# Kernel optimization log

Hardware: AMD Instinct MI355X
Metric: run time of the kernel (lower is better)

The kernel has to match this reference:

```python
import jax, jax.numpy as jnp
import numpy as np

B, K, D, E = 8192, 5, 128, 128
QD = D + 1              # query_dim = embedding_dimension + time_encoding_dim(=1)
KD = K * (D + E + 1)    # flattened neighborhood feature width = key_dim*5


def setup_inputs() -> dict:
    key = jax.random.key(0)
    ks = jax.random.split(key, 20)
    n = jax.random.normal
    u = jax.random.uniform
    return {
        # hop-2 neighborhood (neighbors-of-neighbors of B roots)
        "emb0": n(ks[0], (B * K, K, D), jnp.float32),
        "ef0": n(ks[1], (B * K, K, E), jnp.float32),
        "td0": u(ks[2], (B * K, K, 1), jnp.float32),
        # hop-1 neighborhood
        "emb1": n(ks[3], (B, K, D), jnp.float32),
        "ef1": n(ks[4], (B, K, E), jnp.float32),
        "td1": u(ks[5], (B, K, 1), jnp.float32),
        # root embeddings
        "emb2": n(ks[6], (B, D), jnp.float32),
        # single-head MultiheadAttention params (q/k/v in-proj + out-proj)
        "Wq": n(ks[7], (QD, QD), jnp.float32) * 0.05,
        "bq": jnp.zeros((QD,), jnp.float32),
        "Wk": n(ks[8], (QD, KD), jnp.float32) * 0.02,
        "bk": jnp.zeros((QD,), jnp.float32),
        "Wv": n(ks[9], (QD, KD), jnp.float32) * 0.02,
        "bv": jnp.zeros((QD,), jnp.float32),
        "Wo": n(ks[10], (QD, QD), jnp.float32) * 0.05,
        "bo": jnp.zeros((QD,), jnp.float32),
        # fc1: (query_dim + D) -> D, fc2: D -> D
        "W1": n(ks[11], (D, QD + D), jnp.float32) * 0.05,
        "b1": jnp.zeros((D,), jnp.float32),
        "W2": n(ks[12], (D, D), jnp.float32) * 0.05,
        "b2": jnp.zeros((D,), jnp.float32),
    }


def reference(emb0, ef0, td0, emb1, ef1, td1, emb2,
              Wq, bq, Wk, bk, Wv, bv, Wo, bo, W1, b1, W2, b2):
    def attn(q, kv):
        # single-head MHA, batch_first; PyTorch scales q by head_dim**-0.5
        qp = (q @ Wq.T + bq) * (1.0 / jnp.sqrt(jnp.asarray(QD, q.dtype)))
        kp = kv @ Wk.T + bk
        vp = kv @ Wv.T + bv
        w = jax.nn.softmax(jnp.einsum("bqd,bkd->bqk", qp, kp), axis=-1)
        o = jnp.einsum("bqk,bkd->bqd", w, vp)
        return o @ Wo.T + bo

    def mlp(x):
        return jax.nn.relu(x @ W1.T + b1) @ W2.T + b2

    # i = 0: hop-2 neighborhoods attend into hop-1 nodes
    nf0 = jnp.concatenate([emb0, ef0, td0], axis=-1).reshape(B, K, KD)  # [B,K,KD]
    q0 = jnp.concatenate([emb1, td1], axis=-1)                          # [B,K,QD]
    a0 = attn(q0, nf0)
    r0 = mlp(jnp.concatenate([a0, emb1], axis=-1))                      # [B,K,D]

    # i = 1 (last): hop-1 neighborhoods; 2-D root query is reshaped to [1,B,QD]
    # so attention runs across the whole batch, as in the original code.
    nf1 = jnp.concatenate([emb1, ef1, td1], axis=-1).reshape(1, B, KD)  # [1,B,KD]
    q1 = jnp.concatenate([emb2, jnp.zeros((B, 1), emb2.dtype)], axis=-1)[None]
    a1 = attn(q1, nf1)
    r1 = mlp(jnp.concatenate([a1, emb2[None]], axis=-1))[0]             # [B,D]

    return (r0, r1)
```

## Files before the change

kernel.cpp:

```cpp
#include <hip/hip_runtime.h>

#define B_   8192
#define K_   5
#define D_   128
#define QD_  129
#define KD_  1285
#define SQ_  132
#define BK_  40960
#define QPAD 160
#define VPAD 144
#define KDP  1312

typedef unsigned short u16;
typedef unsigned int   u32;
typedef __attribute__((ext_vector_type(8))) short bf8_t;
typedef __attribute__((ext_vector_type(4))) float f4_t;
typedef __attribute__((address_space(3))) u32 lds_u32;
typedef __attribute__((address_space(1))) const u32 glob_u32;

#define MFMA16(a, b, c) __builtin_amdgcn_mfma_f32_16x16x32_bf16(a, b, c, 0, 0, 0)

__device__ __forceinline__ u16 f2bf(float x) {
  u32 u = __float_as_uint(x);
  u = (u + 0x7fffu + ((u >> 16) & 1u)) >> 16;
  return (u16)u;
}
__device__ __forceinline__ float bf2f(u16 v) {
  return __uint_as_float((u32)v << 16);
}
__device__ __forceinline__ u32 pack2(float a, float b) {
  return (u32)f2bf(a) | ((u32)f2bf(b) << 16);
}
__device__ __forceinline__ float exp2_fast(float x) {
#if __has_builtin(__builtin_amdgcn_exp2f)
  return __builtin_amdgcn_exp2f(x);
#else
  float r; asm("v_exp_f32 %0, %1" : "=v"(r) : "v"(x)); return r;
#endif
}
__device__ __forceinline__ u32 cvtpk(float a, float b) {
  u32 r;
  asm("v_cvt_pk_bf16_f32 %0, %1, %2" : "=v"(r) : "v"(a), "v"(b));
  return r;
}
__device__ __forceinline__ int swz8(int row, int seg) {
  return (row << 5) + (((seg ^ (row >> 1)) & 3) << 3);
}
__device__ __forceinline__ void gload16(const u16* src, u16* ldsdst) {
  __builtin_amdgcn_global_load_lds((glob_u32*)src, (lds_u32*)ldsdst, 16, 0, 0);
}
#define WAIT_VM0() asm volatile("s_waitcnt vmcnt(0)" ::: "memory")
#define WAIT_VM3() asm volatile("s_waitcnt vmcnt(3)" ::: "memory")
#define WAIT_VM4() asm volatile("s_waitcnt vmcnt(4)" ::: "memory")
#define WAIT_VM6() asm volatile("s_waitcnt vmcnt(6)" ::: "memory")
#define WAIT_LGKM0() asm volatile("s_waitcnt lgkmcnt(0)" ::: "memory")

__global__ __launch_bounds__(256) void convw_k(
    const float* __restrict__ Wq, const float* __restrict__ Wk,
    const float* __restrict__ Wv, const float* __restrict__ Wo,
    const float* __restrict__ W1, const float* __restrict__ W2,
    u16* __restrict__ wb)
{
  int idx = blockIdx.x * 256 + threadIdx.x;
  if (idx < 377856) {
    int r = idx / KDP, c = idx - r * KDP;
    float v = 0.f;
    if (c < KD_) {
      if (r < 129) v = Wk[r * KD_ + c];
      else if (r < 258) v = Wv[(r - 129) * KD_ + c];
    }
    wb[idx] = f2bf(v);
    return;
  }
  int i2 = idx - 377856;
  if (i2 < 23040) {
    int r = i2 / 160, c = i2 - r * 160;
    wb[idx] = f2bf((r < 129 && c < 129) ? Wq[r * 129 + c] : 0.f);
    return;
  }
  i2 -= 23040;
  if (i2 < 23040) {
    int r = i2 / 160, c = i2 - r * 160;
    wb[idx] = f2bf((r < 129 && c < 129) ? Wo[r * 129 + c] : 0.f);
    return;
  }
  i2 -= 23040;
  if (i2 < 41472) {
    int r = i2 / 288, c = i2 - r * 288;
    wb[idx] = f2bf((r < 128 && c < 257) ? W1[r * 257 + c] : 0.f);
    return;
  }
  i2 -= 41472;
  if (i2 < 18432) {
    int r = i2 / 128, c = i2 - r * 128;
    wb[idx] = f2bf(r < 128 ? W2[r * 128 + c] : 0.f);
  }
}

__global__ __launch_bounds__(256) void packnf_k(
    const float* __restrict__ emb, const float* __restrict__ ef,
    const float* __restrict__ td, u16* __restrict__ dst, int nofs, int rows)
{
  int idx = blockIdx.x * 256 + threadIdx.x;
  if (idx >= rows * 328) return;
  int nr = idx / 328, q = idx - nr * 328;
  const int n = nofs + nr;
  const int c0 = q * 4;
  u16 o[4];
#pragma unroll
  for (int i = 0; i < 4; ++i) {
    int c = c0 + i;
    float v = 0.f;
    if (c < KD_) {
      int j = c / 257, r = c - j * 257;
      int base = (n * 5 + j) << 7;
      v = (r < 128) ? emb[base + r] : (r < 256) ? ef[base + r - 128] : td[n * 5 + j];
    }
    o[i] = f2bf(v);
  }
  *(uint2*)&dst[(size_t)nr * KDP + c0] = *(const uint2*)o;
}

template<int GA, bool RELU, int OM0, int OM1, bool DUAL>
__global__ __launch_bounds__(256) void gmm_k(
    int nK, int Kw, int nch,
    const void* __restrict__ A, int ast,
    const float* __restrict__ g1, const float* __restrict__ g2,
    const u16* __restrict__ Wb,
    const float* __restrict__ b0, void* __restrict__ out0, int ost0, int N0,
    const float* __restrict__ b1, void* __restrict__ out1, int ost1,
    float scale)
{
  __shared__ u16 Ws_[3][9 * 512];
  const int t = threadIdx.x, lane = t & 63, w = t >> 6;
  const int lrow = lane & 15, lk = lane >> 4;
  const int bid = blockIdx.x;
  const int x = bid / nch, colh = bid - x * nch;
  const int n0 = x * 64;
  const int colofs = colh * 144;
  const int drow = lane >> 2, dseg = lane & 3;
  const int arow = n0 + w * 16 + lrow;

  f4_t acc[9];
#pragma unroll
  for (int ct = 0; ct < 9; ++ct) acc[ct] = (f4_t){0.f, 0.f, 0.f, 0.f};

  bf8_t afE, afO;
  float rE[8], rO[8];

  auto issueR = [&](int kst, float (&r)[8]) {
    const int cb = kst * 32 + lk * 8;
#pragma unroll
    for (int i = 0; i < 8; ++i) {
      int c = cb + i;
      uintptr_t pa = (uintptr_t)((const float*)A + (arow << 7) + c);
      uintptr_t pt = (uintptr_t)(g2 ? (g2 + arow) : (const float*)A);
      uintptr_t sel = (c < 128) ? pa : pt;
      float v = *(const float*)sel;
      r[i] = (c < 128) ? v : ((c == 128 && g2) ? v : 0.f);
    }
  };
  auto cvt8 = [&](const float (&r)[8]) -> bf8_t {
    union { bf8_t v; u32 u[4]; } xx;
#pragma unroll
    for (int i = 0; i < 4; ++i) xx.u[i] = pack2(r[2 * i], r[2 * i + 1]);
    return xx.v;
  };
  auto loadAf = [&](int kst) -> bf8_t {
    return *(const bf8_t*)((const u16*)A + (size_t)arow * ast + kst * 32 + lk * 8);
  };
  auto dmaW = [&](int kst, u16* wbuf) {
    const int c0 = kst * 32;
#pragma unroll
    for (int si = 0; si < 3; ++si) {
      int s = w + si * 4;
      if (s < 9) {
        int rr = colofs + s * 16 + drow;
        int sseg = (dseg ^ (rr >> 1)) & 3;
        gload16(&Wb[(size_t)rr * Kw + c0 + sseg * 8], wbuf + s * 512);
      }
    }
  };
  auto compute = [&](bf8_t af, const u16* wsb) {
#pragma unroll
    for (int ct = 0; ct < 9; ++ct) {
      bf8_t bf = *(const bf8_t*)&wsb[swz8(ct * 16 + lrow, lk)];
      acc[ct] = MFMA16(af, bf, acc[ct]);
    }
  };

  if constexpr (GA == 0) {
    u16 *wa = Ws_[0], *wbuf = Ws_[1], *wc = Ws_[2];
    afE = loadAf(0);
    dmaW(0, wa);
    if (nK > 1) { afO = loadAf(1); dmaW(1, wbuf); }
    if (nK > 1) { WAIT_VM4(); } else { WAIT_VM0(); }
    __builtin_amdgcn_s_barrier();
    int k = 0;
    while (true) {
      if (k + 2 < nK) dmaW(k + 2, wc);
      compute(afE, wa);
      if (k + 2 < nK) afE = loadAf(k + 2);
      if (k + 1 >= nK) break;
      if (k + 2 < nK) { WAIT_VM4(); } else { WAIT_VM0(); }
      __builtin_amdgcn_s_barrier();
      { u16* tp = wa; wa = wbuf; wbuf = wc; wc = tp; }
      ++k;
      if (k + 2 < nK) dmaW(k + 2, wc);
      compute(afO, wa);
      if (k + 2 < nK) afO = loadAf(k + 2);
      if (k + 1 >= nK) break;
      if (k + 2 < nK) { WAIT_VM4(); } else { WAIT_VM0(); }
      __builtin_amdgcn_s_barrier();
      { u16* tp = wa; wa = wbuf; wbuf = wc; wc = tp; }
      ++k;
    }
  } else {
    issueR(0, rE);
    dmaW(0, Ws_[0]);
    WAIT_VM0();
    afE = cvt8(rE);
    __builtin_amdgcn_s_barrier();
    int cur = 0, k = 0;
    while (true) {
      if (k + 1 < nK) { issueR(k + 1, rO); dmaW(k + 1, Ws_[cur ^ 1]); }
      compute(afE, Ws_[cur]);
      if (k + 1 >= nK) break;
      WAIT_VM0();
      afO = cvt8(rO);
      __builtin_amdgcn_s_barrier();
      cur ^= 1; ++k;
      if (k + 1 < nK) { issueR(k + 1, rE); dmaW(k + 1, Ws_[cur ^ 1]); }
      compute(afO, Ws_[cur]);
      if (k + 1 >= nK) break;
      WAIT_VM0();
      afE = cvt8(rE);
      __builtin_amdgcn_s_barrier();
      cur ^= 1; ++k;
    }
  }

#pragma unroll
  for (int ct = 0; ct < 9; ++ct) {
    const int col = colofs + ct * 16 + lrow;
#pragma unroll
    for (int r = 0; r < 4; ++r) {
      const int n = n0 + w * 16 + lk * 4 + r;
      float v = acc[ct][r];
      if (col < N0) {
        v = (v + b0[col]) * scale;
        if (RELU) v = fmaxf(v, 0.f);
        if (OM0 == 0)      ((float*)out0)[(size_t)n * ost0 + col] = v;
        else if (OM0 == 1) ((u16*)out0)[(size_t)n * ost0 + col] = f2bf(v);
        else               ((u16*)out0)[(size_t)col * ost0 + n] = f2bf(v);
      } else if (DUAL) {
        int o = col - N0;
        if (o < 129) {
          v = (v + b1[o]) * scale;
          if (RELU) v = fmaxf(v, 0.f);
          if (OM1 == 0)      ((float*)out1)[(size_t)n * ost1 + o] = v;
          else if (OM1 == 1) ((u16*)out1)[(size_t)n * ost1 + o] = f2bf(v);
          else               ((u16*)out1)[(size_t)o * ost1 + n] = f2bf(v);
        }
      }
    }
  }
}

__global__ __launch_bounds__(256) void embpack_k(
    const float* __restrict__ src, u16* __restrict__ dst, int rows)
{
  int idx = blockIdx.x * 256 + threadIdx.x;
  if (idx >= rows * 128) return;
  int n = idx >> 7, c = idx & 127;
  dst[(size_t)n * 288 + 129 + c] = f2bf(src[idx]);
}

__global__ __launch_bounds__(256) void attn0_k(
    const u16* __restrict__ qp, const u16* __restrict__ kp,
    const u16* __restrict__ vp, u16* __restrict__ o0b)
{
  __shared__ float qs[4][5][SQ_], ks[4][5][SQ_], vs[4][5][SQ_];
  __shared__ float ps[4][5][8];
  const int t = threadIdx.x;
  const int bbase = blockIdx.x * 4;
  for (int idx = t; idx < 4 * 5 * 33; idx += 256) {
    int bl = idx / 165;
    int rem = idx - bl * 165;
    int row = rem / 33;
    int g = rem - row * 33;
    int n = (bbase + bl) * 5 + row;
    int d0 = g * 4;
    uint2 uq = *(const uint2*)&qp[(size_t)n * 160 + d0];
    uint2 uk = *(const uint2*)&kp[(size_t)n * 160 + d0];
    uint2 uv = *(const uint2*)&vp[(size_t)n * 160 + d0];
    u16 eq[4] = {(u16)uq.x, (u16)(uq.x >> 16), (u16)uq.y, (u16)(uq.y >> 16)};
    u16 ek[4] = {(u16)uk.x, (u16)(uk.x >> 16), (u16)uk.y, (u16)(uk.y >> 16)};
    u16 ev[4] = {(u16)uv.x, (u16)(uv.x >> 16), (u16)uv.y, (u16)(uv.y >> 16)};
#pragma unroll
    for (int i = 0; i < 4; ++i) {
      int d = d0 + i;
      bool ok = d < QD_;
      qs[bl][row][d] = ok ? bf2f(eq[i]) : 0.f;
      ks[bl][row][d] = ok ? bf2f(ek[i]) : 0.f;
      vs[bl][row][d] = ok ? bf2f(ev[i]) : 0.f;
    }
  }
  __syncthreads();
  const int w = t >> 6, lane = t & 63;
  if (lane < 25) {
    int qq = lane / 5, kk = lane - (lane / 5) * 5;
    float s = 0.f;
    for (int c = 0; c < SQ_; c += 4) {
      float4 qv = *(const float4*)&qs[w][qq][c];
      float4 kv = *(const float4*)&ks[w][kk][c];
      s += qv.x * kv.x + qv.y * kv.y + qv.z * kv.z + qv.w * kv.w;
    }
    ps[w][qq][kk] = s;
  }
  __syncthreads();
  if (lane < 5) {
    float m = -1e30f;
#pragma unroll
    for (int k = 0; k < 5; ++k) m = fmaxf(m, ps[w][lane][k]);
    float l = 0.f; float e[5];
#pragma unroll
    for (int k = 0; k < 5; ++k) { e[k] = __expf(ps[w][lane][k] - m); l += e[k]; }
    float inv = 1.f / l;
#pragma unroll
    for (int k = 0; k < 5; ++k) ps[w][lane][k] = e[k] * inv;
  }
  __syncthreads();
  for (int d = lane; d < 160; d += 64) {
#pragma unroll
    for (int qq = 0; qq < 5; ++qq) {
      float o = 0.f;
      if (d < QD_) {
#pragma unroll
        for (int k = 0; k < 5; ++k) o += ps[w][qq][k] * vs[w][k][d];
      }
      o0b[(size_t)((bbase + w) * 5 + qq) * 160 + d] = f2bf(o);
    }
  }
}

#define QB   128
#define KVB  64
#define NSPLIT 8
#define NT   ((B_ / NSPLIT) / KVB)
__global__ __launch_bounds__(512, 4) void flashm_k(
    const u16* __restrict__ qp, const u16* __restrict__ kp,
    const u16* __restrict__ vpT, float* __restrict__ oacc,
    float* __restrict__ marr, float* __restrict__ larr)
{
  __shared__ u16 Ks[2][5 * 2048];
  __shared__ u16 Vs[2 * 4608];
  __shared__ u16 Ps[2 * 4096];
  const int t = threadIdx.x, lane = t & 63, w = t >> 6;
  const int lrow = lane & 15, lk = lane >> 4;
  const int split = blockIdx.x & (NSPLIT - 1);
  const int q0 = (blockIdx.x >> 3) * QB;
  const int drow = lane >> 2, dseg = lane & 3;
  const int kbase = split * (B_ / NSPLIT);

  auto dmaK = [&](int k0, u16* kb) {
#pragma unroll
    for (int si = 0; si < 3; ++si) {
      int s = w + si * 8;
      if (s >= 20) s -= 20;
      int kst = s >> 2, rg = s & 3;
      int r = rg * 16 + drow;
      int sseg = (dseg ^ (r >> 1)) & 3;
      gload16(&kp[(size_t)(k0 + r) * QPAD + kst * 32 + sseg * 8],
              kb + kst * 2048 + rg * 512);
    }
  };
  auto dmaV = [&](int k0) {
#pragma unroll
    for (int si = 0; si < 3; ++si) {
      int s = w + si * 8;
      if (s >= 18) s -= 18;
      int kst = (s >= 9) ? 1 : 0;
      int rg = s - kst * 9;
      int r = rg * 16 + drow;
      int sseg = (dseg ^ (r >> 1)) & 3;
      gload16(&vpT[(size_t)r * B_ + k0 + kst * 32 + sseg * 8],
              Vs + kst * 4608 + rg * 512);
    }
  };

  bf8_t qf[5];
  {
    const u16* qrow = qp + (size_t)(q0 + w * 16 + lrow) * QPAD;
#pragma unroll
    for (int kst = 0; kst < 5; ++kst)
      qf[kst] = *(const bf8_t*)(qrow + kst * 32 + lk * 8);
  }

  f4_t acc[9];
#pragma unroll
  for (int ct = 0; ct < 9; ++ct) acc[ct] = (f4_t){0.f, 0.f, 0.f, 0.f};
  float m_[4] = {-1e30f, -1e30f, -1e30f, -1e30f};
  float l_[4] = {0.f, 0.f, 0.f, 0.f};

  dmaK(kbase, Ks[0]);
  for (int tl = 0; tl < NT; ++tl) {
    const int k0 = kbase + tl * KVB;
    const int cur = tl & 1;
    dmaV(k0);
    const bool more = (tl + 1 < NT);
    if (more) dmaK(k0 + KVB, Ks[cur ^ 1]);
    if (more) { WAIT_VM6(); } else { WAIT_VM3(); }
    __builtin_amdgcn_s_barrier();

    f4_t s4[4];
#pragma unroll
    for (int ct = 0; ct < 4; ++ct) s4[ct] = (f4_t){0.f, 0.f, 0.f, 0.f};
#pragma unroll
    for (int kst = 0; kst < 5; ++kst) {
#pragma unroll
      for (int ct = 0; ct < 4; ++ct) {
        bf8_t b = *(const bf8_t*)&Ks[cur][kst * 2048 + swz8(ct * 16 + lrow, lk)];
        s4[ct] = MFMA16(qf[kst], b, s4[ct]);
      }
    }

    float lmax[4];
#pragma unroll
    for (int r = 0; r < 4; ++r)
      lmax[r] = fmaxf(fmaxf(s4[0][r], s4[1][r]), fmaxf(s4[2][r], s4[3][r]));
    bool need = (lmax[0] > m_[0] + 8.f) || (lmax[1] > m_[1] + 8.f) ||
                (lmax[2] > m_[2] + 8.f) || (lmax[3] > m_[3] + 8.f);
    if (__any(need)) {
      float cf[4];
#pragma unroll
      for (int r = 0; r < 4; ++r) {
        float pm = lmax[r];
#pragma unroll
        for (int mk = 1; mk <= 8; mk <<= 1) pm = fmaxf(pm, __shfl_xor(pm, mk));
        float mn = fmaxf(m_[r], pm);
        cf[r] = exp2_fast(m_[r] - mn);
        m_[r] = mn;
        l_[r] *= cf[r];
      }
#pragma unroll
      for (int ct = 0; ct < 9; ++ct) {
#pragma unroll
        for (int r = 0; r < 4; ++r) acc[ct][r] *= cf[r];
      }
    }
    float pv[4][4];
#pragma unroll
    for (int ct = 0; ct < 4; ++ct) {
#pragma unroll
      for (int r = 0; r < 4; ++r) {
        pv[ct][r] = exp2_fast(s4[ct][r] - m_[r]);
        l_[r] += pv[ct][r];
      }
    }
#pragma unroll
    for (int half = 0; half < 2; ++half) {
#pragma unroll
      for (int r = 0; r < 4; ++r) {
        u32 pk = cvtpk(pv[half * 2][r], pv[half * 2 + 1][r]);
        const int q = w * 16 + lk * 4 + r;
        const int c0 = lrow, c1 = 16 + lrow;
        const int base = half * 4096 + (q << 5);
        Ps[base + ((((c0 >> 3) ^ (q >> 1)) & 3) << 3) + (c0 & 7)] = (u16)pk;
        Ps[base + ((((c1 >> 3) ^ (q >> 1)) & 3) << 3) + (c1 & 7)] = (u16)(pk >> 16);
      }
    }
    WAIT_LGKM0();
    __builtin_amdgcn_sched_barrier(0);

    if (more) { WAIT_VM3(); } else { WAIT_VM0(); }
    __builtin_amdgcn_s_barrier();

#pragma unroll
    for (int kst = 0; kst < 2; ++kst) {
      bf8_t a = *(const bf8_t*)&Ps[kst * 4096 + swz8(w * 16 + lrow, lk)];
#pragma unroll
      for (int ct = 0; ct < 9; ++ct) {
        bf8_t b = *(const bf8_t*)&Vs[kst * 4608 + swz8(ct * 16 + lrow, lk)];
        acc[ct] = MFMA16(a, b, acc[ct]);
      }
    }
    __builtin_amdgcn_s_barrier();
  }

#pragma unroll
  for (int r = 0; r < 4; ++r) {
#pragma unroll
    for (int mk = 1; mk <= 8; mk <<= 1) l_[r] += __shfl_xor(l_[r], mk);
  }

#pragma unroll
  for (int ct = 0; ct < 9; ++ct) {
    const int col = ct * 16 + lrow;
    if (col < SQ_) {
#pragma unroll
      for (int r = 0; r < 4; ++r)
        oacc[((size_t)split * B_ + q0 + w * 16 + lk * 4 + r) * SQ_ + col] = acc[ct][r];
    }
  }
  if (lrow == 0) {
#pragma unroll
    for (int r = 0; r < 4; ++r) {
      size_t i = (size_t)split * B_ + q0 + w * 16 + lk * 4 + r;
      marr[i] = m_[r];
      larr[i] = l_[r];
    }
  }
}

__global__ __launch_bounds__(256) void combine_k(
    const float* __restrict__ oacc, const float* __restrict__ marr,
    const float* __restrict__ larr, u16* __restrict__ o1b)
{
  int idx = blockIdx.x * 256 + threadIdx.x;
  if (idx >= B_ * 160) return;
  int n = idx / 160, d = idx - n * 160;
  float v = 0.f;
  if (d < QD_) {
    float m = -1e30f;
#pragma unroll
    for (int s = 0; s < NSPLIT; ++s) m = fmaxf(m, marr[s * B_ + n]);
    float l = 0.f, o = 0.f;
#pragma unroll
    for (int s = 0; s < NSPLIT; ++s) {
      float e = exp2_fast(marr[s * B_ + n] - m);
      l += larr[s * B_ + n] * e;
      o += oacc[((size_t)s * B_ + n) * SQ_ + d] * e;
    }
    v = o / l;
  }
  o1b[idx] = f2bf(v);
}

extern "C" void kernel_launch(void* const* d_in, const int* in_sizes, int n_in,
                              void* d_out, int out_size, void* d_ws, size_t ws_size,
                              hipStream_t stream)
{
  const float* emb0 = (const float*)d_in[0];
  const float* ef0  = (const float*)d_in[1];
  const float* td0  = (const float*)d_in[2];
  const float* emb1 = (const float*)d_in[3];
  const float* ef1  = (const float*)d_in[4];
  const float* td1  = (const float*)d_in[5];
  const float* emb2 = (const float*)d_in[6];
  const float* Wq = (const float*)d_in[7];  const float* bq = (const float*)d_in[8];
  const float* Wk = (const float*)d_in[9];  const float* bk = (const float*)d_in[10];
  const float* Wv = (const float*)d_in[11]; const float* bv = (const float*)d_in[12];
  const float* Wo = (const float*)d_in[13]; const float* bo = (const float*)d_in[14];
  const float* W1 = (const float*)d_in[15]; const float* b1 = (const float*)d_in[16];
  const float* W2 = (const float*)d_in[17]; const float* b2 = (const float*)d_in[18];
  float* out = (float*)d_out;

  char* ws = (char*)d_ws;
  u16* wb   = (u16*)ws;
  u16* wkv  = wb;
  u16* wq_b = wb + 377856;
  u16* wo_b = wb + 400896;
  u16* w1_b = wb + 423936;
  u16* w2_b = wb + 465408;
  u16*   kp0b = (u16*)(ws + 1048576);
  u16*   vp0b = (u16*)(ws + 14155776);
  u16*   qp0b = (u16*)(ws + 27262976);
  u16*   nfp  = (u16*)(ws + 44302336);
  u16*   o0b  = (u16*)(ws + 65929216);
  u16*   cat0 = (u16*)(ws + 1048576);
  u16*   h0   = (u16*)(ws + 24641536);
  u16*   nf1p = (u16*)(ws + 1048576);
  u16*   qp1b = (u16*)(ws + 22675456);
  u16*   kp1b = (u16*)(ws + 25296896);
  u16*   vp1T = (u16*)(ws + 27918336);
  u16*   o1b  = (u16*)(ws + 30277632);
  float* marr = (float*)(ws + 32899072);
  float* larr = (float*)(ws + 33161216);
  u16*   cat1 = (u16*)(ws + 33423360);
  u16*   h1   = (u16*)(ws + 38141952);
  float* oacc = (float*)(ws + 40239104);

  const float scale = 0.08804509063256238f;
  const float scale2 = scale * 1.4426950408889634f;
  const int HROWS = 20480;

  convw_k<<<1890, 256, 0, stream>>>(Wq, Wk, Wv, Wo, W1, W2, wb);

  for (int h = 0; h < 2; ++h) {
    packnf_k<<<(HROWS * 328 + 255) / 256, 256, 0, stream>>>(
        emb0, ef0, td0, nfp, h * HROWS, HROWS);
    gmm_k<0, false, 1, 1, true><<<(HROWS / 64) * 2, 256, 0, stream>>>(
        41, KDP, 2, nfp, KDP, nullptr, nullptr, wkv,
        bk, kp0b + (size_t)h * HROWS * 160, 160, QD_,
        bv, vp0b + (size_t)h * HROWS * 160, 160, 1.f);
  }
  gmm_k<1, false, 1, 0, false><<<640, 256, 0, stream>>>(
      5, 160, 1, emb1, 0, nullptr, td1, wq_b,
      bq, qp0b, 160, QD_, nullptr, nullptr, 0, scale);
  attn0_k<<<B_ / 4, 256, 0, stream>>>(qp0b, kp0b, vp0b, o0b);
  hipMemsetAsync(cat0, 0, 23592960, stream);
  embpack_k<<<(BK_ * 128 + 255) / 256, 256, 0, stream>>>(emb1, cat0, BK_);
  gmm_k<0, false, 1, 0, false><<<640, 256, 0, stream>>>(
      5, 160, 1, o0b, 160, nullptr, nullptr, wo_b,
      bo, cat0, 288, QD_, nullptr, nullptr, 0, 1.f);
  gmm_k<0, true, 1, 0, false><<<640, 256, 0, stream>>>(
      9, 288, 1, cat0, 288, nullptr, nullptr, w1_b,
      b1, h0, 128, 128, nullptr, nullptr, 0, 1.f);
  gmm_k<0, false, 0, 0, false><<<640, 256, 0, stream>>>(
      4, 128, 1, h0, 128, nullptr, nullptr, w2_b,
      b2, out, 128, 128, nullptr, nullptr, 0, 1.f);

  packnf_k<<<(B_ * 328 + 255) / 256, 256, 0, stream>>>(
      emb1, ef1, td1, nf1p, 0, B_);
  hipMemsetAsync(qp1b, 0, 2621440, stream);
  hipMemsetAsync(kp1b, 0, 2621440, stream);
  hipMemsetAsync(vp1T, 0, 2359296, stream);
  gmm_k<0, false, 1, 2, true><<<(B_ / 64) * 2, 256, 0, stream>>>(
      41, KDP, 2, nf1p, KDP, nullptr, nullptr, wkv,
      bk, kp1b, QPAD, QD_, bv, vp1T, B_, 1.f);
  gmm_k<1, false, 1, 0, false><<<128, 256, 0, stream>>>(
      5, 160, 1, emb2, 0, nullptr, nullptr, wq_b,
      bq, qp1b, QPAD, QD_, nullptr, nullptr, 0, scale2);
  flashm_k<<<(B_ / QB) * NSPLIT, 512, 0, stream>>>(qp1b, kp1b, vp1T, oacc, marr, larr);
  combine_k<<<(B_ * 160 + 255) / 256, 256, 0, stream>>>(oacc, marr, larr, o1b);
  hipMemsetAsync(cat1, 0, 4718592, stream);
  embpack_k<<<(B_ * 128 + 255) / 256, 256, 0, stream>>>(emb2, cat1, B_);
  gmm_k<0, false, 1, 0, false><<<128, 256, 0, stream>>>(
      5, 160, 1, o1b, 160, nullptr, nullptr, wo_b,
      bo, cat1, 288, QD_, nullptr, nullptr, 0, 1.f);
  gmm_k<0, true, 1, 0, false><<<128, 256, 0, stream>>>(
      9, 288, 1, cat1, 288, nullptr, nullptr, w1_b,
      b1, h1, 128, 128, nullptr, nullptr, 0, 1.f);
  gmm_k<0, false, 0, 0, false><<<128, 256, 0, stream>>>(
      4, 128, 1, h1, 128, nullptr, nullptr, w2_b,
      b2, out + (size_t)BK_ * D_, 128, 128, nullptr, nullptr, 0, 1.f);
}
```

Baseline: 416.2 us.

## Fuse concat into fc1 GEMM and rewrite flash attention with 32x32 MFMA

The fc1 GEMM now reads its A operand from two sources: the bf16 attention output (padded to 160) and the fp32 embeddings, converting the latter on the fly. This removes the memset and embpack kernels that used to build the concatenated buffer, and the W1 layout is repacked to 320 columns to match. Separately, the cross-batch flash attention kernel moves from 16x16x32 MFMA with 512-thread blocks to 32x32x16 MFMA with 256-thread blocks and 32 query rows per wave, giving more reuse per instruction. The cost is higher register pressure (16 row stats per lane) and a wider K step in fc1.

```diff
diff --git a/kernel.cpp b/kernel.cpp
--- a/kernel.cpp
+++ b/kernel.cpp
@@ -8,17 +8,18 @@
 #define SQ_  132
 #define BK_  40960
 #define QPAD 160
-#define VPAD 144
 #define KDP  1312
 
 typedef unsigned short u16;
 typedef unsigned int   u32;
 typedef __attribute__((ext_vector_type(8))) short bf8_t;
 typedef __attribute__((ext_vector_type(4))) float f4_t;
+typedef __attribute__((ext_vector_type(16))) float f16f;
 typedef __attribute__((address_space(3))) u32 lds_u32;
 typedef __attribute__((address_space(1))) const u32 glob_u32;
 
 #define MFMA16(a, b, c) __builtin_amdgcn_mfma_f32_16x16x32_bf16(a, b, c, 0, 0, 0)
+#define MFMA32(a, b, c) __builtin_amdgcn_mfma_f32_32x32x16_bf16(a, b, c, 0, 0, 0)
 
 __device__ __forceinline__ u16 f2bf(float x) {
   u32 u = __float_as_uint(x);
@@ -32,11 +33,7 @@
   return (u32)f2bf(a) | ((u32)f2bf(b) << 16);
 }
 __device__ __forceinline__ float exp2_fast(float x) {
-#if __has_builtin(__builtin_amdgcn_exp2f)
-  return __builtin_amdgcn_exp2f(x);
-#else
   float r; asm("v_exp_f32 %0, %1" : "=v"(r) : "v"(x)); return r;
-#endif
 }
 __device__ __forceinline__ u32 cvtpk(float a, float b) {
   u32 r;
@@ -50,9 +47,9 @@
   __builtin_amdgcn_global_load_lds((glob_u32*)src, (lds_u32*)ldsdst, 16, 0, 0);
 }
 #define WAIT_VM0() asm volatile("s_waitcnt vmcnt(0)" ::: "memory")
-#define WAIT_VM3() asm volatile("s_waitcnt vmcnt(3)" ::: "memory")
 #define WAIT_VM4() asm volatile("s_waitcnt vmcnt(4)" ::: "memory")
-#define WAIT_VM6() asm volatile("s_waitcnt vmcnt(6)" ::: "memory")
+#define WAIT_VM5() asm volatile("s_waitcnt vmcnt(5)" ::: "memory")
+#define WAIT_VM10() asm volatile("s_waitcnt vmcnt(10)" ::: "memory")
 #define WAIT_LGKM0() asm volatile("s_waitcnt lgkmcnt(0)" ::: "memory")
 
 __global__ __launch_bounds__(256) void convw_k(
@@ -85,12 +82,17 @@
     return;
   }
   i2 -= 23040;
-  if (i2 < 41472) {
-    int r = i2 / 288, c = i2 - r * 288;
-    wb[idx] = f2bf((r < 128 && c < 257) ? W1[r * 257 + c] : 0.f);
+  if (i2 < 46080) {
+    int r = i2 / 320, c = i2 - r * 320;
+    float v = 0.f;
+    if (r < 128) {
+      if (c < 129) v = W1[r * 257 + c];
+      else if (c >= 160 && c < 288) v = W1[r * 257 + (c - 31)];
+    }
+    wb[idx] = f2bf(v);
     return;
   }
-  i2 -= 41472;
+  i2 -= 46080;
   if (i2 < 18432) {
     int r = i2 / 128, c = i2 - r * 128;
     wb[idx] = f2bf(r < 128 ? W2[r * 128 + c] : 0.f);
@@ -121,7 +123,7 @@
   *(uint2*)&dst[(size_t)nr * KDP + c0] = *(const uint2*)o;
 }
 
-template<int GA, bool RELU, int OM0, int OM1, bool DUAL>
+template<int GA, bool RELU, int OM0, int OM1, bool DUAL, bool ZF = false>
 __global__ __launch_bounds__(256) void gmm_k(
     int nK, int Kw, int nch,
     const void* __restrict__ A, int ast,
@@ -145,7 +147,7 @@
 #pragma unroll
   for (int ct = 0; ct < 9; ++ct) acc[ct] = (f4_t){0.f, 0.f, 0.f, 0.f};
 
-  bf8_t afE, afO;
+  bf8_t afE, afO, dE, dO;
   float rE[8], rO[8];
 
   auto issueR = [&](int kst, float (&r)[8]) {
@@ -168,6 +170,22 @@
   };
   auto loadAf = [&](int kst) -> bf8_t {
     return *(const bf8_t*)((const u16*)A + (size_t)arow * ast + kst * 32 + lk * 8);
+  };
+  auto issue2 = [&](int kst, bf8_t& d, float (&r)[8]) {
+    if (GA == 1) { issueR(kst, r); return; }
+    if (kst < 5) { d = loadAf(kst); }
+    else if (kst < 9) {
+      const float* p = g1 + (size_t)arow * 128 + (kst - 5) * 32 + lk * 8;
+      *(float4*)&r[0] = *(const float4*)p;
+      *(float4*)&r[4] = *(const float4*)(p + 4);
+    }
+  };
+  auto finish2 = [&](int kst, bf8_t& d, float (&r)[8]) -> bf8_t {
+    if (GA == 1) return cvt8(r);
+    if (kst < 5) return d;
+    if (kst < 9) return cvt8(r);
+    bf8_t z = {0, 0, 0, 0, 0, 0, 0, 0};
+    return z;
   };
   auto dmaW = [&](int kst, u16* wbuf) {
     const int c0 = kst * 32;
@@ -216,25 +234,25 @@
       ++k;
     }
   } else {
-    issueR(0, rE);
+    issue2(0, dE, rE);
     dmaW(0, Ws_[0]);
     WAIT_VM0();
-    afE = cvt8(rE);
+    afE = finish2(0, dE, rE);
     __builtin_amdgcn_s_barrier();
     int cur = 0, k = 0;
     while (true) {
-      if (k + 1 < nK) { issueR(k + 1, rO); dmaW(k + 1, Ws_[cur ^ 1]); }
+      if (k + 1 < nK) { issue2(k + 1, dO, rO); dmaW(k + 1, Ws_[cur ^ 1]); }
       compute(afE, Ws_[cur]);
       if (k + 1 >= nK) break;
       WAIT_VM0();
-      afO = cvt8(rO);
+      afO = finish2(k + 1, dO, rO);
       __builtin_amdgcn_s_barrier();
       cur ^= 1; ++k;
-      if (k + 1 < nK) { issueR(k + 1, rE); dmaW(k + 1, Ws_[cur ^ 1]); }
+      if (k + 1 < nK) { issue2(k + 1, dE, rE); dmaW(k + 1, Ws_[cur ^ 1]); }
       compute(afO, Ws_[cur]);
       if (k + 1 >= nK) break;
       WAIT_VM0();
-      afE = cvt8(rE);
+      afE = finish2(k + 1, dE, rE);
       __builtin_amdgcn_s_barrier();
       cur ^= 1; ++k;
     }
@@ -262,18 +280,11 @@
           else if (OM1 == 1) ((u16*)out1)[(size_t)n * ost1 + o] = f2bf(v);
           else               ((u16*)out1)[(size_t)o * ost1 + n] = f2bf(v);
         }
+      } else if (ZF && col < 144) {
+        if (OM0 == 1) ((u16*)out0)[(size_t)n * ost0 + col] = 0;
       }
     }
   }
-}
-
-__global__ __launch_bounds__(256) void embpack_k(
-    const float* __restrict__ src, u16* __restrict__ dst, int rows)
-{
-  int idx = blockIdx.x * 256 + threadIdx.x;
-  if (idx >= rows * 128) return;
-  int n = idx >> 7, c = idx & 127;
-  dst[(size_t)n * 288 + 129 + c] = f2bf(src[idx]);
 }
 
 __global__ __launch_bounds__(256) void attn0_k(
@@ -348,16 +359,16 @@
 #define KVB  64
 #define NSPLIT 8
 #define NT   ((B_ / NSPLIT) / KVB)
-__global__ __launch_bounds__(512, 4) void flashm_k(
+__global__ __launch_bounds__(256, 2) void flashm_k(
     const u16* __restrict__ qp, const u16* __restrict__ kp,
     const u16* __restrict__ vpT, float* __restrict__ oacc,
     float* __restrict__ marr, float* __restrict__ larr)
 {
   __shared__ u16 Ks[2][5 * 2048];
-  __shared__ u16 Vs[2 * 4608];
-  __shared__ u16 Ps[2 * 4096];
+  __shared__ u16 Vs[2 * 5120];
+  __shared__ u16 Ps[4 * 2048];
   const int t = threadIdx.x, lane = t & 63, w = t >> 6;
-  const int lrow = lane & 15, lk = lane >> 4;
+  const int l31 = lane & 31, lh = lane >> 5;
   const int split = blockIdx.x & (NSPLIT - 1);
   const int q0 = (blockIdx.x >> 3) * QB;
   const int drow = lane >> 2, dseg = lane & 3;
@@ -365,9 +376,8 @@
 
   auto dmaK = [&](int k0, u16* kb) {
 #pragma unroll
-    for (int si = 0; si < 3; ++si) {
-      int s = w + si * 8;
-      if (s >= 20) s -= 20;
+    for (int si = 0; si < 5; ++si) {
+      int s = w + si * 4;
       int kst = s >> 2, rg = s & 3;
       int r = rg * 16 + drow;
       int sseg = (dseg ^ (r >> 1)) & 3;
@@ -377,31 +387,41 @@
   };
   auto dmaV = [&](int k0) {
 #pragma unroll
-    for (int si = 0; si < 3; ++si) {
-      int s = w + si * 8;
+    for (int si = 0; si < 5; ++si) {
+      int s = w + si * 4;
       if (s >= 18) s -= 18;
       int kst = (s >= 9) ? 1 : 0;
       int rg = s - kst * 9;
       int r = rg * 16 + drow;
       int sseg = (dseg ^ (r >> 1)) & 3;
       gload16(&vpT[(size_t)r * B_ + k0 + kst * 32 + sseg * 8],
-              Vs + kst * 4608 + rg * 512);
-    }
-  };
-
-  bf8_t qf[5];
+              Vs + kst * 5120 + rg * 512);
+    }
+  };
+
+  bf8_t qf[10];
   {
-    const u16* qrow = qp + (size_t)(q0 + w * 16 + lrow) * QPAD;
-#pragma unroll
-    for (int kst = 0; kst < 5; ++kst)
-      qf[kst] = *(const bf8_t*)(qrow + kst * 32 + lk * 8);
-  }
-
-  f4_t acc[9];
-#pragma unroll
-  for (int ct = 0; ct < 9; ++ct) acc[ct] = (f4_t){0.f, 0.f, 0.f, 0.f};
-  float m_[4] = {-1e30f, -1e30f, -1e30f, -1e30f};
-  float l_[4] = {0.f, 0.f, 0.f, 0.f};
+    const u16* qrow = qp + (size_t)(q0 + w * 32 + l31) * QPAD;
+#pragma unroll
+    for (int kst = 0; kst < 10; ++kst)
+      qf[kst] = *(const bf8_t*)(qrow + kst * 16 + lh * 8);
+  }
+
+  f16f acc[5];
+#pragma unroll
+  for (int ct = 0; ct < 5; ++ct)
+#pragma unroll
+    for (int j = 0; j < 16; ++j) acc[ct][j] = 0.f;
+  float m_[16], l_[16];
+#pragma unroll
+  for (int r = 0; r < 16; ++r) { m_[r] = -1e30f; l_[r] = 0.f; }
+
+  int paddr[16];
+#pragma unroll
+  for (int r = 0; r < 16; ++r) {
+    int q = (r & 3) + 8 * (r >> 2) + 4 * lh;
+    paddr[r] = w * 2048 + (q << 5) + ((((l31 >> 3) ^ (q >> 1)) & 3) << 3) + (l31 & 7);
+  }
 
   dmaK(kbase, Ks[0]);
   for (int tl = 0; tl < NT; ++tl) {
@@ -410,103 +430,92 @@
     dmaV(k0);
     const bool more = (tl + 1 < NT);
     if (more) dmaK(k0 + KVB, Ks[cur ^ 1]);
-    if (more) { WAIT_VM6(); } else { WAIT_VM3(); }
+    if (more) { WAIT_VM10(); } else { WAIT_VM5(); }
     __builtin_amdgcn_s_barrier();
 
-    f4_t s4[4];
-#pragma unroll
-    for (int ct = 0; ct < 4; ++ct) s4[ct] = (f4_t){0.f, 0.f, 0.f, 0.f};
-#pragma unroll
-    for (int kst = 0; kst < 5; ++kst) {
-#pragma unroll
-      for (int ct = 0; ct < 4; ++ct) {
-        bf8_t b = *(const bf8_t*)&Ks[cur][kst * 2048 + swz8(ct * 16 + lrow, lk)];
-        s4[ct] = MFMA16(qf[kst], b, s4[ct]);
+    f16f s0, s1;
+#pragma unroll
+    for (int j = 0; j < 16; ++j) { s0[j] = 0.f; s1[j] = 0.f; }
+#pragma unroll
+    for (int kst = 0; kst < 10; ++kst) {
+      const int seg = ((kst & 1) << 1) + lh;
+      bf8_t b0 = *(const bf8_t*)&Ks[cur][(kst >> 1) * 2048 + swz8(l31, seg)];
+      bf8_t b1 = *(const bf8_t*)&Ks[cur][(kst >> 1) * 2048 + swz8(32 + l31, seg)];
+      s0 = MFMA32(qf[kst], b0, s0);
+      s1 = MFMA32(qf[kst], b1, s1);
+    }
+
+    float lm[16];
+    bool need = false;
+#pragma unroll
+    for (int r = 0; r < 16; ++r) {
+      lm[r] = fmaxf(s0[r], s1[r]);
+      need = need || (lm[r] > m_[r] + 8.f);
+    }
+    if (__any(need)) {
+#pragma unroll
+      for (int r = 0; r < 16; ++r) {
+        float pm = lm[r];
+#pragma unroll
+        for (int mk = 1; mk <= 16; mk <<= 1) pm = fmaxf(pm, __shfl_xor(pm, mk));
+        float mn = fmaxf(m_[r], pm);
+        float cf = exp2_fast(m_[r] - mn);
+        m_[r] = mn;
+        l_[r] *= cf;
+#pragma unroll
+        for (int ct = 0; ct < 5; ++ct) acc[ct][r] *= cf;
       }
     }
-
-    float lmax[4];
-#pragma unroll
-    for (int r = 0; r < 4; ++r)
-      lmax[r] = fmaxf(fmaxf(s4[0][r], s4[1][r]), fmaxf(s4[2][r], s4[3][r]));
-    bool need = (lmax[0] > m_[0] + 8.f) || (lmax[1] > m_[1] + 8.f) ||
-                (lmax[2] > m_[2] + 8.f) || (lmax[3] > m_[3] + 8.f);
-    if (__any(need)) {
-      float cf[4];
-#pragma unroll
-      for (int r = 0; r < 4; ++r) {
-        float pm = lmax[r];
-#pragma unroll
-        for (int mk = 1; mk <= 8; mk <<= 1) pm = fmaxf(pm, __shfl_xor(pm, mk));
-        float mn = fmaxf(m_[r], pm);
-        cf[r] = exp2_fast(m_[r] - mn);
-        m_[r] = mn;
-        l_[r] *= cf[r];
-      }
-#pragma unroll
-      for (int ct = 0; ct < 9; ++ct) {
-#pragma unroll
-        for (int r = 0; r < 4; ++r) acc[ct][r] *= cf[r];
-      }
-    }
-    float pv[4][4];
-#pragma unroll
-    for (int ct = 0; ct < 4; ++ct) {
-#pragma unroll
-      for (int r = 0; r < 4; ++r) {
-        pv[ct][r] = exp2_fast(s4[ct][r] - m_[r]);
-        l_[r] += pv[ct][r];
-      }
-    }
-#pragma unroll
-    for (int half = 0; half < 2; ++half) {
-#pragma unroll
-      for (int r = 0; r < 4; ++r) {
-        u32 pk = cvtpk(pv[half * 2][r], pv[half * 2 + 1][r]);
-        const int q = w * 16 + lk * 4 + r;
-        const int c0 = lrow, c1 = 16 + lrow;
-        const int base = half * 4096 + (q << 5);
-        Ps[base + ((((c0 >> 3) ^ (q >> 1)) & 3) << 3) + (c0 & 7)] = (u16)pk;
-        Ps[base + ((((c1 >> 3) ^ (q >> 1)) & 3) << 3) + (c1 & 7)] = (u16)(pk >> 16);
-      }
+#pragma unroll
+    for (int r = 0; r < 16; ++r) {
+      float p0 = exp2_fast(s0[r] - m_[r]);
+      float p1 = exp2_fast(s1[r] - m_[r]);
+      l_[r] += p0 + p1;
+      u32 pk = cvtpk(p0, p1);
+      Ps[paddr[r]] = (u16)pk;
+      Ps[paddr[r] + 1024] = (u16)(pk >> 16);
     }
     WAIT_LGKM0();
     __builtin_amdgcn_sched_barrier(0);
 
-    if (more) { WAIT_VM3(); } else { WAIT_VM0(); }
+    if (more) { WAIT_VM5(); } else { WAIT_VM0(); }
     __builtin_amdgcn_s_barrier();
 
 #pragma unroll
-    for (int kst = 0; kst < 2; ++kst) {
-      bf8_t a = *(const bf8_t*)&Ps[kst * 4096 + swz8(w * 16 + lrow, lk)];
-#pragma unroll
-      for (int ct = 0; ct < 9; ++ct) {
-        bf8_t b = *(const bf8_t*)&Vs[kst * 4608 + swz8(ct * 16 + lrow, lk)];
-        acc[ct] = MFMA16(a, b, acc[ct]);
+    for (int kst = 0; kst < 4; ++kst) {
+      const int seg = ((kst & 1) << 1) + lh;
+      bf8_t a = *(const bf8_t*)&Ps[w * 2048 + (kst >> 1) * 1024 + swz8(l31, seg)];
+#pragma unroll
+      for (int ct = 0; ct < 5; ++ct) {
+        bf8_t b = *(const bf8_t*)&Vs[(kst >> 1) * 5120 + swz8(ct * 32 + l31, seg)];
+        acc[ct] = MFMA32(a, b, acc[ct]);
       }
     }
     __builtin_amdgcn_s_barrier();
   }
 
 #pragma unroll
-  for (int r = 0; r < 4; ++r) {
-#pragma unroll
-    for (int mk = 1; mk <= 8; mk <<= 1) l_[r] += __shfl_xor(l_[r], mk);
-  }
-
-#pragma unroll
-  for (int ct = 0; ct < 9; ++ct) {
-    const int col = ct * 16 + lrow;
+  for (int r = 0; r < 16; ++r) {
+#pragma unroll
+    for (int mk = 1; mk <= 16; mk <<= 1) l_[r] += __shfl_xor(l_[r], mk);
+  }
+
+#pragma unroll
+  for (int ct = 0; ct < 5; ++ct) {
+    const int col = ct * 32 + l31;
     if (col < SQ_) {
 #pragma unroll
-      for (int r = 0; r < 4; ++r)
-        oacc[((size_t)split * B_ + q0 + w * 16 + lk * 4 + r) * SQ_ + col] = acc[ct][r];
-    }
-  }
-  if (lrow == 0) {
-#pragma unroll
-    for (int r = 0; r < 4; ++r) {
-      size_t i = (size_t)split * B_ + q0 + w * 16 + lk * 4 + r;
+      for (int r = 0; r < 16; ++r) {
+        const int q = q0 + w * 32 + (r & 3) + 8 * (r >> 2) + 4 * lh;
+        oacc[((size_t)split * B_ + q) * SQ_ + col] = acc[ct][r];
+      }
+    }
+  }
+  if (l31 == 0) {
+#pragma unroll
+    for (int r = 0; r < 16; ++r) {
+      const int q = q0 + w * 32 + (r & 3) + 8 * (r >> 2) + 4 * lh;
+      size_t i = (size_t)split * B_ + q;
       marr[i] = m_[r];
       larr[i] = l_[r];
     }
@@ -562,13 +571,13 @@
   u16* wq_b = wb + 377856;
   u16* wo_b = wb + 400896;
   u16* w1_b = wb + 423936;
-  u16* w2_b = wb + 465408;
+  u16* w2_b = wb + 470016;
   u16*   kp0b = (u16*)(ws + 1048576);
   u16*   vp0b = (u16*)(ws + 14155776);
   u16*   qp0b = (u16*)(ws + 27262976);
   u16*   nfp  = (u16*)(ws + 44302336);
   u16*   o0b  = (u16*)(ws + 65929216);
-  u16*   cat0 = (u16*)(ws + 1048576);
+  u16*   a1b0 = (u16*)(ws + 1048576);
   u16*   h0   = (u16*)(ws + 24641536);
   u16*   nf1p = (u16*)(ws + 1048576);
   u16*   qp1b = (u16*)(ws + 22675456);
@@ -577,7 +586,7 @@
   u16*   o1b  = (u16*)(ws + 30277632);
   float* marr = (float*)(ws + 32899072);
   float* larr = (float*)(ws + 33161216);
-  u16*   cat1 = (u16*)(ws + 33423360);
+  u16*   a1b1 = (u16*)(ws + 33423360);
   u16*   h1   = (u16*)(ws + 38141952);
   float* oacc = (float*)(ws + 40239104);
 
@@ -585,7 +594,7 @@
   const float scale2 = scale * 1.4426950408889634f;
   const int HROWS = 20480;
 
-  convw_k<<<1890, 256, 0, stream>>>(Wq, Wk, Wv, Wo, W1, W2, wb);
+  convw_k<<<1908, 256, 0, stream>>>(Wq, Wk, Wv, Wo, W1, W2, wb);
 
   for (int h = 0; h < 2; ++h) {
     packnf_k<<<(HROWS * 328 + 255) / 256, 256, 0, stream>>>(
@@ -599,13 +608,11 @@
       5, 160, 1, emb1, 0, nullptr, td1, wq_b,
       bq, qp0b, 160, QD_, nullptr, nullptr, 0, scale);
   attn0_k<<<B_ / 4, 256, 0, stream>>>(qp0b, kp0b, vp0b, o0b);
-  hipMemsetAsync(cat0, 0, 23592960, stream);
-  embpack_k<<<(BK_ * 128 + 255) / 256, 256, 0, stream>>>(emb1, cat0, BK_);
-  gmm_k<0, false, 1, 0, false><<<640, 256, 0, stream>>>(
+  gmm_k<0, false, 1, 0, false, true><<<640, 256, 0, stream>>>(
       5, 160, 1, o0b, 160, nullptr, nullptr, wo_b,
-      bo, cat0, 288, QD_, nullptr, nullptr, 0, 1.f);
-  gmm_k<0, true, 1, 0, false><<<640, 256, 0, stream>>>(
-      9, 288, 1, cat0, 288, nullptr, nullptr, w1_b,
+      bo, a1b0, 160, QD_, nullptr, nullptr, 0, 1.f);
+  gmm_k<2, true, 1, 0, false><<<640, 256, 0, stream>>>(
+      10, 320, 1, a1b0, 160, emb1, nullptr, w1_b,
       b1, h0, 128, 128, nullptr, nullptr, 0, 1.f);
   gmm_k<0, false, 0, 0, false><<<640, 256, 0, stream>>>(
       4, 128, 1, h0, 128, nullptr, nullptr, w2_b,
@@ -622,15 +629,13 @@
   gmm_k<1, false, 1, 0, false><<<128, 256, 0, stream>>>(
       5, 160, 1, emb2, 0, nullptr, nullptr, wq_b,
       bq, qp1b, QPAD, QD_, nullptr, nullptr, 0, scale2);
-  flashm_k<<<(B_ / QB) * NSPLIT, 512, 0, stream>>>(qp1b, kp1b, vp1T, oacc, marr, larr);
+  flashm_k<<<(B_ / QB) * NSPLIT, 256, 0, stream>>>(qp1b, kp1b, vp1T, oacc, marr, larr);
   combine_k<<<(B_ * 160 + 255) / 256, 256, 0, stream>>>(oacc, marr, larr, o1b);
-  hipMemsetAsync(cat1, 0, 4718592, stream);
-  embpack_k<<<(B_ * 128 + 255) / 256, 256, 0, stream>>>(emb2, cat1, B_);
-  gmm_k<0, false, 1, 0, false><<<128, 256, 0, stream>>>(
+  gmm_k<0, false, 1, 0, false, true><<<128, 256, 0, stream>>>(
       5, 160, 1, o1b, 160, nullptr, nullptr, wo_b,
-      bo, cat1, 288, QD_, nullptr, nullptr, 0, 1.f);
-  gmm_k<0, true, 1, 0, false><<<128, 256, 0, stream>>>(
-      9, 288, 1, cat1, 288, nullptr, nullptr, w1_b,
+      bo, a1b1, 160, QD_, nullptr, nullptr, 0, 1.f);
+  gmm_k<2, true, 1, 0, false><<<128, 256, 0, stream>>>(
+      10, 320, 1, a1b1, 160, emb2, nullptr, w1_b,
       b1, h1, 128, 128, nullptr, nullptr, 0, 1.f);
   gmm_k<0, false, 0, 0, false><<<128, 256, 0, stream>>>(
       4, 128, 1, h1, 128, nullptr, nullptr, w2_b,
```

Measured after the change: 429.4 us. +3.2%, slower.

## Fuse MLP input concat into fc1 GEMM and store flash partials as bf16

Applied to the files above, without the earlier changes.

The concat buffers and their memsets and embpack kernels are removed. Instead, the fc1 GEMM reads the attention output (bf16, padded to 160) for its first 5 k-steps and the fp32 embeddings directly for the next 4, converting them to bf16 in registers. W1 is repacked to match this 320-wide layout, and the out-proj GEMM zero-fills its padding columns. Separately, the flash-attention split partial accumulators are now stored as bf16 instead of fp32, which halves combine traffic at some cost in precision.

```diff
diff --git a/kernel.cpp b/kernel.cpp
--- a/kernel.cpp
+++ b/kernel.cpp
@@ -32,11 +32,7 @@
   return (u32)f2bf(a) | ((u32)f2bf(b) << 16);
 }
 __device__ __forceinline__ float exp2_fast(float x) {
-#if __has_builtin(__builtin_amdgcn_exp2f)
-  return __builtin_amdgcn_exp2f(x);
-#else
   float r; asm("v_exp_f32 %0, %1" : "=v"(r) : "v"(x)); return r;
-#endif
 }
 __device__ __forceinline__ u32 cvtpk(float a, float b) {
   u32 r;
@@ -85,12 +81,17 @@
     return;
   }
   i2 -= 23040;
-  if (i2 < 41472) {
-    int r = i2 / 288, c = i2 - r * 288;
-    wb[idx] = f2bf((r < 128 && c < 257) ? W1[r * 257 + c] : 0.f);
+  if (i2 < 46080) {
+    int r = i2 / 320, c = i2 - r * 320;
+    float v = 0.f;
+    if (r < 128) {
+      if (c < 129) v = W1[r * 257 + c];
+      else if (c >= 160 && c < 288) v = W1[r * 257 + (c - 31)];
+    }
+    wb[idx] = f2bf(v);
     return;
   }
-  i2 -= 41472;
+  i2 -= 46080;
   if (i2 < 18432) {
     int r = i2 / 128, c = i2 - r * 128;
     wb[idx] = f2bf(r < 128 ? W2[r * 128 + c] : 0.f);
@@ -121,7 +122,7 @@
   *(uint2*)&dst[(size_t)nr * KDP + c0] = *(const uint2*)o;
 }
 
-template<int GA, bool RELU, int OM0, int OM1, bool DUAL>
+template<int GA, bool RELU, int OM0, int OM1, bool DUAL, bool ZF = false>
 __global__ __launch_bounds__(256) void gmm_k(
     int nK, int Kw, int nch,
     const void* __restrict__ A, int ast,
@@ -145,7 +146,7 @@
 #pragma unroll
   for (int ct = 0; ct < 9; ++ct) acc[ct] = (f4_t){0.f, 0.f, 0.f, 0.f};
 
-  bf8_t afE, afO;
+  bf8_t afE, afO, dE, dO;
   float rE[8], rO[8];
 
   auto issueR = [&](int kst, float (&r)[8]) {
@@ -168,6 +169,22 @@
   };
   auto loadAf = [&](int kst) -> bf8_t {
     return *(const bf8_t*)((const u16*)A + (size_t)arow * ast + kst * 32 + lk * 8);
+  };
+  auto issue2 = [&](int kst, bf8_t& d, float (&r)[8]) {
+    if (GA == 1) { issueR(kst, r); return; }
+    if (kst < 5) { d = loadAf(kst); }
+    else if (kst < 9) {
+      const float* p = g1 + (size_t)arow * 128 + (kst - 5) * 32 + lk * 8;
+      *(float4*)&r[0] = *(const float4*)p;
+      *(float4*)&r[4] = *(const float4*)(p + 4);
+    }
+  };
+  auto finish2 = [&](int kst, bf8_t& d, float (&r)[8]) -> bf8_t {
+    if (GA == 1) return cvt8(r);
+    if (kst < 5) return d;
+    if (kst < 9) return cvt8(r);
+    bf8_t z = {0, 0, 0, 0, 0, 0, 0, 0};
+    return z;
   };
   auto dmaW = [&](int kst, u16* wbuf) {
     const int c0 = kst * 32;
@@ -216,25 +233,25 @@
       ++k;
     }
   } else {
-    issueR(0, rE);
+    issue2(0, dE, rE);
     dmaW(0, Ws_[0]);
     WAIT_VM0();
-    afE = cvt8(rE);
+    afE = finish2(0, dE, rE);
     __builtin_amdgcn_s_barrier();
     int cur = 0, k = 0;
     while (true) {
-      if (k + 1 < nK) { issueR(k + 1, rO); dmaW(k + 1, Ws_[cur ^ 1]); }
+      if (k + 1 < nK) { issue2(k + 1, dO, rO); dmaW(k + 1, Ws_[cur ^ 1]); }
       compute(afE, Ws_[cur]);
       if (k + 1 >= nK) break;
       WAIT_VM0();
-      afO = cvt8(rO);
+      afO = finish2(k + 1, dO, rO);
       __builtin_amdgcn_s_barrier();
       cur ^= 1; ++k;
-      if (k + 1 < nK) { issueR(k + 1, rE); dmaW(k + 1, Ws_[cur ^ 1]); }
+      if (k + 1 < nK) { issue2(k + 1, dE, rE); dmaW(k + 1, Ws_[cur ^ 1]); }
       compute(afO, Ws_[cur]);
       if (k + 1 >= nK) break;
       WAIT_VM0();
-      afE = cvt8(rE);
+      afE = finish2(k + 1, dE, rE);
       __builtin_amdgcn_s_barrier();
       cur ^= 1; ++k;
     }
@@ -262,18 +279,11 @@
           else if (OM1 == 1) ((u16*)out1)[(size_t)n * ost1 + o] = f2bf(v);
           else               ((u16*)out1)[(size_t)o * ost1 + n] = f2bf(v);
         }
-      }
-    }
-  }
-}
-
-__global__ __launch_bounds__(256) void embpack_k(
-    const float* __restrict__ src, u16* __restrict__ dst, int rows)
-{
-  int idx = blockIdx.x * 256 + threadIdx.x;
-  if (idx >= rows * 128) return;
-  int n = idx >> 7, c = idx & 127;
-  dst[(size_t)n * 288 + 129 + c] = f2bf(src[idx]);
+      } else if (ZF && col < 144) {
+        if (OM0 == 1) ((u16*)out0)[(size_t)n * ost0 + col] = 0;
+      }
+    }
+  }
 }
 
 __global__ __launch_bounds__(256) void attn0_k(
@@ -350,7 +360,7 @@
 #define NT   ((B_ / NSPLIT) / KVB)
 __global__ __launch_bounds__(512, 4) void flashm_k(
     const u16* __restrict__ qp, const u16* __restrict__ kp,
-    const u16* __restrict__ vpT, float* __restrict__ oacc,
+    const u16* __restrict__ vpT, u16* __restrict__ oacc,
     float* __restrict__ marr, float* __restrict__ larr)
 {
   __shared__ u16 Ks[2][5 * 2048];
@@ -500,7 +510,7 @@
     if (col < SQ_) {
 #pragma unroll
       for (int r = 0; r < 4; ++r)
-        oacc[((size_t)split * B_ + q0 + w * 16 + lk * 4 + r) * SQ_ + col] = acc[ct][r];
+        oacc[((size_t)split * B_ + q0 + w * 16 + lk * 4 + r) * SQ_ + col] = f2bf(acc[ct][r]);
     }
   }
   if (lrow == 0) {
@@ -514,7 +524,7 @@
 }
 
 __global__ __launch_bounds__(256) void combine_k(
-    const float* __restrict__ oacc, const float* __restrict__ marr,
+    const u16* __restrict__ oacc, const float* __restrict__ marr,
     const float* __restrict__ larr, u16* __restrict__ o1b)
 {
   int idx = blockIdx.x * 256 + threadIdx.x;
@@ -530,7 +540,7 @@
     for (int s = 0; s < NSPLIT; ++s) {
       float e = exp2_fast(marr[s * B_ + n] - m);
       l += larr[s * B_ + n] * e;
-      o += oacc[((size_t)s * B_ + n) * SQ_ + d] * e;
+      o += bf2f(oacc[((size_t)s * B_ + n) * SQ_ + d]) * e;
     }
     v = o / l;
   }
@@ -562,13 +572,13 @@
   u16* wq_b = wb + 377856;
   u16* wo_b = wb + 400896;
   u16* w1_b = wb + 423936;
-  u16* w2_b = wb + 465408;
+  u16* w2_b = wb + 470016;
   u16*   kp0b = (u16*)(ws + 1048576);
   u16*   vp0b = (u16*)(ws + 14155776);
   u16*   qp0b = (u16*)(ws + 27262976);
   u16*   nfp  = (u16*)(ws + 44302336);
   u16*   o0b  = (u16*)(ws + 65929216);
-  u16*   cat0 = (u16*)(ws + 1048576);
+  u16*   a1b0 = (u16*)(ws + 1048576);
   u16*   h0   = (u16*)(ws + 24641536);
   u16*   nf1p = (u16*)(ws + 1048576);
   u16*   qp1b = (u16*)(ws + 22675456);
@@ -577,15 +587,15 @@
   u16*   o1b  = (u16*)(ws + 30277632);
   float* marr = (float*)(ws + 32899072);
   float* larr = (float*)(ws + 33161216);
-  u16*   cat1 = (u16*)(ws + 33423360);
+  u16*   a1b1 = (u16*)(ws + 33423360);
   u16*   h1   = (u16*)(ws + 38141952);
-  float* oacc = (float*)(ws + 40239104);
+  u16*   oacc = (u16*)(ws + 40239104);
 
   const float scale = 0.08804509063256238f;
   const float scale2 = scale * 1.4426950408889634f;
   const int HROWS = 20480;
 
-  convw_k<<<1890, 256, 0, stream>>>(Wq, Wk, Wv, Wo, W1, W2, wb);
+  convw_k<<<1908, 256, 0, stream>>>(Wq, Wk, Wv, Wo, W1, W2, wb);
 
   for (int h = 0; h < 2; ++h) {
     packnf_k<<<(HROWS * 328 + 255) / 256, 256, 0, stream>>>(
@@ -599,13 +609,11 @@
       5, 160, 1, emb1, 0, nullptr, td1, wq_b,
       bq, qp0b, 160, QD_, nullptr, nullptr, 0, scale);
   attn0_k<<<B_ / 4, 256, 0, stream>>>(qp0b, kp0b, vp0b, o0b);
-  hipMemsetAsync(cat0, 0, 23592960, stream);
-  embpack_k<<<(BK_ * 128 + 255) / 256, 256, 0, stream>>>(emb1, cat0, BK_);
-  gmm_k<0, false, 1, 0, false><<<640, 256, 0, stream>>>(
+  gmm_k<0, false, 1, 0, false, true><<<640, 256, 0, stream>>>(
       5, 160, 1, o0b, 160, nullptr, nullptr, wo_b,
-      bo, cat0, 288, QD_, nullptr, nullptr, 0, 1.f);
-  gmm_k<0, true, 1, 0, false><<<640, 256, 0, stream>>>(
-      9, 288, 1, cat0, 288, nullptr, nullptr, w1_b,
+      bo, a1b0, 160, QD_, nullptr, nullptr, 0, 1.f);
+  gmm_k<2, true, 1, 0, false><<<640, 256, 0, stream>>>(
+      10, 320, 1, a1b0, 160, emb1, nullptr, w1_b,
       b1, h0, 128, 128, nullptr, nullptr, 0, 1.f);
   gmm_k<0, false, 0, 0, false><<<640, 256, 0, stream>>>(
       4, 128, 1, h0, 128, nullptr, nullptr, w2_b,
@@ -624,13 +632,11 @@
       bq, qp1b, QPAD, QD_, nullptr, nullptr, 0, scale2);
   flashm_k<<<(B_ / QB) * NSPLIT, 512, 0, stream>>>(qp1b, kp1b, vp1T, oacc, marr, larr);
   combine_k<<<(B_ * 160 + 255) / 256, 256, 0, stream>>>(oacc, marr, larr, o1b);
-  hipMemsetAsync(cat1, 0, 4718592, stream);
-  embpack_k<<<(B_ * 128 + 255) / 256, 256, 0, stream>>>(emb2, cat1, B_);
-  gmm_k<0, false, 1, 0, false><<<128, 256, 0, stream>>>(
+  gmm_k<0, false, 1, 0, false, true><<<128, 256, 0, stream>>>(
       5, 160, 1, o1b, 160, nullptr, nullptr, wo_b,
-      bo, cat1, 288, QD_, nullptr, nullptr, 0, 1.f);
-  gmm_k<0, true, 1, 0, false><<<128, 256, 0, stream>>>(
-      9, 288, 1, cat1, 288, nullptr, nullptr, w1_b,
+      bo, a1b1, 160, QD_, nullptr, nullptr, 0, 1.f);
+  gmm_k<2, true, 1, 0, false><<<128, 256, 0, stream>>>(
+      10, 320, 1, a1b1, 160, emb2, nullptr, w1_b,
       b1, h1, 128, 128, nullptr, nullptr, 0, 1.f);
   gmm_k<0, false, 0, 0, false><<<128, 256, 0, stream>>>(
       4, 128, 1, h1, 128, nullptr, nullptr, w2_b,
```

New measurement: 404.4 us. -2.9%, faster.
